# Kernel optimization log

Measured on AMD Instinct MI355X. Metric: run time of the kernel, lower is better.

## Reference

```python
import jax, jax.numpy as jnp
import numpy as np

N, P, E, HID = 20000, 12, 640000, 100

def setup_inputs() -> dict:
    key = jax.random.key(0)
    ks = jax.random.split(key, 20)
    inp = {}
    inp['x'] = jax.random.normal(ks[0], (N, P), dtype=jnp.float32)
    inp['edge_index'] = jax.random.randint(ks[1], (2, E), 0, N, dtype=jnp.int64)
    inp['edge_weight'] = jax.random.uniform(ks[2], (E,), dtype=jnp.float32)
    s = 0.1
    # GCNConv weights (in=1, out=HID) and biases for z, r, h gates
    inp['W_z'] = jax.random.normal(ks[3], (1, HID)) * s
    inp['b_z'] = jnp.zeros((HID,))
    inp['W_r'] = jax.random.normal(ks[4], (1, HID)) * s
    inp['b_r'] = jnp.zeros((HID,))
    inp['W_h'] = jax.random.normal(ks[5], (1, HID)) * s
    inp['b_h'] = jnp.zeros((HID,))
    # TGCN linear layers: Linear(2*HID, HID), stored as (in, out)
    inp['Wl_z'] = jax.random.normal(ks[6], (2 * HID, HID)) * s
    inp['bl_z'] = jnp.zeros((HID,))
    inp['Wl_r'] = jax.random.normal(ks[7], (2 * HID, HID)) * s
    inp['bl_r'] = jnp.zeros((HID,))
    inp['Wl_h'] = jax.random.normal(ks[8], (2 * HID, HID)) * s
    inp['bl_h'] = jnp.zeros((HID,))
    # A3TGCN temporal attention logits over periods
    inp['att'] = jax.random.uniform(ks[9], (P,))
    # final Linear(100, 1)
    inp['W_out'] = jax.random.normal(ks[10], (HID, 1)) * s
    inp['b_out'] = jnp.zeros((1,))
    return inp

def _gcn_aggregate(x_np, edge_index, edge_weight):
    # symmetric GCN normalization with self-loops (PyG gcn_norm), then
    # aggregate neighbor features: out[i] = sum_j norm_ij * x[j]
    n = x_np.shape[0]
    src, dst = edge_index[0], edge_index[1]
    loop = jnp.arange(n)
    s = jnp.concatenate([src, loop])
    d = jnp.concatenate([dst, loop])
    w = jnp.concatenate([edge_weight, jnp.ones((n,), dtype=x_np.dtype)])
    deg = jax.ops.segment_sum(w, d, num_segments=n)
    dinv = jnp.where(deg > 0, deg ** -0.5, 0.0)
    norm = dinv[s] * w * dinv[d]                      # (E+N,)
    msgs = norm[:, None] * x_np[s]                    # (E+N, P)
    return jax.ops.segment_sum(msgs, d, num_segments=n)  # (N, P)

def reference(x, edge_index, edge_weight, W_z, b_z, W_r, b_r, W_h, b_h,
              Wl_z, bl_z, Wl_r, bl_r, Wl_h, bl_h, att, W_out, b_out):
    # x: (N, P) -> viewed as (N, in_channels=1, P) in the torch module.
    # GCNConv is linear in x, so aggregate once and apply each gate's weight.
    agg = _gcn_aggregate(x, edge_index, edge_weight)       # (N, P)
    C_z = agg[:, :, None] * W_z[0] + b_z                   # (N, P, HID)
    C_r = agg[:, :, None] * W_r[0] + b_r
    C_h = agg[:, :, None] * W_h[0] + b_h
    # A3TGCN calls TGCN with H=None (zeros) for every period independently.
    H0 = jnp.zeros_like(C_z)
    Z = jax.nn.sigmoid(jnp.concatenate([C_z, H0], -1) @ Wl_z + bl_z)
    R = jax.nn.sigmoid(jnp.concatenate([C_r, H0], -1) @ Wl_r + bl_r)
    Ht = jnp.tanh(jnp.concatenate([C_h, H0 * R], -1) @ Wl_h + bl_h)
    Hp = Z * H0 + (1.0 - Z) * Ht                           # (N, P, HID)
    probs = jax.nn.softmax(att)                            # (P,)
    H_acc = jnp.einsum('npo,p->no', Hp, probs)             # (N, HID)
    h = jax.nn.relu(H_acc)
    return h @ W_out + b_out                               # (N, 1)
```

## Files before the change

kernel.cpp:

```cpp
#include <hip/hip_runtime.h>
#include <hip/hip_bf16.h>

constexpr int N_NODES = 20000;
constexpr int P_PER   = 12;
constexpr int N_EDGES = 640000;
constexpr int HID     = 100;
constexpr int CAP     = 80;

constexpr size_t OFF_DINV   = 0;
constexpr size_t OFF_UZ     = OFF_DINV + N_NODES;
constexpr size_t OFF_CZ     = OFF_UZ + HID;
constexpr size_t OFF_UH     = OFF_CZ + HID;
constexpr size_t OFF_CH     = OFF_UH + HID;
constexpr size_t OFF_PROBS  = OFF_CH + HID;
constexpr size_t OFF_CNT    = OFF_PROBS + P_PER;
constexpr size_t OFF_BUCKET = OFF_CNT + N_NODES;

__global__ void precompute_kernel(const float* __restrict__ Wz, const float* __restrict__ bz,
                                  const float* __restrict__ Wh, const float* __restrict__ bh,
                                  const float* __restrict__ Wlz, const float* __restrict__ blz,
                                  const float* __restrict__ Wlh, const float* __restrict__ blh,
                                  const float* __restrict__ att,
                                  float* __restrict__ uz, float* __restrict__ cz,
                                  float* __restrict__ uh, float* __restrict__ ch,
                                  float* __restrict__ probs) {
    int t = threadIdx.x;
    if (t < HID) {
        float suz = 0.f, scz = 0.f, suh = 0.f, sch = 0.f;
        for (int j = 0; j < HID; ++j) {
            float wlz = Wlz[j * HID + t];
            float wlh = Wlh[j * HID + t];
            suz += Wz[j] * wlz;
            scz += bz[j] * wlz;
            suh += Wh[j] * wlh;
            sch += bh[j] * wlh;
        }
        uz[t] = suz;
        cz[t] = scz + blz[t];
        uh[t] = suh;
        ch[t] = sch + blh[t];
    }
    if (t == 0) {
        float m = att[0];
        for (int p = 1; p < P_PER; ++p) m = fmaxf(m, att[p]);
        float e[P_PER];
        float s = 0.f;
        for (int p = 0; p < P_PER; ++p) { e[p] = __expf(att[p] - m); s += e[p]; }
        float inv = 1.0f / s;
        for (int p = 0; p < P_PER; ++p) probs[p] = e[p] * inv;
    }
}

__global__ void fill_bucket_kernel(const int* __restrict__ ei, const float* __restrict__ w,
                                   int* __restrict__ cnt, int2* __restrict__ bucket) {
    int e = blockIdx.x * blockDim.x + threadIdx.x;
    if (e >= N_EDGES) return;
    int s = ei[e];
    int d = ei[N_EDGES + e];
    float wt = w[e];
    int pos = atomicAdd(cnt + d, 1);
    if (pos < CAP) bucket[(size_t)d * CAP + pos] = make_int2(s, __float_as_int(wt));
}

__global__ void degdinv_kernel(const int2* __restrict__ bucket, const int* __restrict__ cnt,
                               float* __restrict__ dinv) {
    int tid = blockIdx.x * blockDim.x + threadIdx.x;
    int n = tid >> 4;
    int l = tid & 15;
    if (n >= N_NODES) return;
    int c = min(cnt[n], CAP);
    const int2* row = bucket + (size_t)n * CAP;
    float s = 0.f;
    for (int j = l; j < c; j += 16) s += __int_as_float(row[j].y);
#pragma unroll
    for (int off = 8; off >= 1; off >>= 1) s += __shfl_xor(s, off, 64);
    if (l == 0) dinv[n] = rsqrtf(1.0f + s);
}

__global__ void gather_finalize_kernel(const int2* __restrict__ bucket, const int* __restrict__ cnt,
                                       const float* __restrict__ x, const float* __restrict__ dinv,
                                       const float* __restrict__ uz, const float* __restrict__ cz,
                                       const float* __restrict__ uh, const float* __restrict__ ch,
                                       const float* __restrict__ probs,
                                       const float* __restrict__ Wout, const float* __restrict__ bout,
                                       float* __restrict__ out) {
    __shared__ float s_uz[HID], s_cz[HID], s_uh[HID], s_ch[HID], s_wo[HID];
    __shared__ float s_pr[P_PER];
    int t = threadIdx.x;
    if (t < HID) {
        s_uz[t] = uz[t]; s_cz[t] = cz[t];
        s_uh[t] = uh[t]; s_ch[t] = ch[t];
        s_wo[t] = Wout[t];
    }
    if (t < P_PER) s_pr[t] = probs[t];
    __syncthreads();

    int tid = blockIdx.x * blockDim.x + t;
    int n = tid >> 4;
    int l = tid & 15;
    if (n >= N_NODES) return;

    int c = min(cnt[n], CAP);
    float dn = dinv[n];
    const int2* row = bucket + (size_t)n * CAP;

    float acc[P_PER];
#pragma unroll
    for (int p = 0; p < P_PER; ++p) acc[p] = 0.f;
    for (int j = l; j < c; j += 16) {
        int2 ent = row[j];
        int s = ent.x;
        float norm = dinv[s] * __int_as_float(ent.y) * dn;
        const float4* xr = (const float4*)(x + (size_t)s * P_PER);
        float4 x0 = xr[0], x1 = xr[1], x2 = xr[2];
        acc[0]  += norm * x0.x;  acc[1]  += norm * x0.y;
        acc[2]  += norm * x0.z;  acc[3]  += norm * x0.w;
        acc[4]  += norm * x1.x;  acc[5]  += norm * x1.y;
        acc[6]  += norm * x1.z;  acc[7]  += norm * x1.w;
        acc[8]  += norm * x2.x;  acc[9]  += norm * x2.y;
        acc[10] += norm * x2.z;  acc[11] += norm * x2.w;
    }
#pragma unroll
    for (int off = 8; off >= 1; off >>= 1) {
#pragma unroll
        for (int p = 0; p < P_PER; ++p) acc[p] += __shfl_xor(acc[p], off, 64);
    }
    {
        const float4* xr = (const float4*)(x + (size_t)n * P_PER);
        float4 x0 = xr[0], x1 = xr[1], x2 = xr[2];
        float self = dn * dn;
        acc[0]  += self * x0.x;  acc[1]  += self * x0.y;
        acc[2]  += self * x0.z;  acc[3]  += self * x0.w;
        acc[4]  += self * x1.x;  acc[5]  += self * x1.y;
        acc[6]  += self * x1.z;  acc[7]  += self * x1.w;
        acc[8]  += self * x2.x;  acc[9]  += self * x2.y;
        acc[10] += self * x2.z;  acc[11] += self * x2.w;
    }
    float rk = 0.f;
    for (int k = l; k < HID; k += 16) {
        float uzk = s_uz[k], czk = s_cz[k], uhk = s_uh[k], chk = s_ch[k];
        float a2 = 0.f;
#pragma unroll
        for (int p = 0; p < P_PER; ++p) {
            float a  = acc[p];
            float vz = fminf(fmaxf(a * uzk + czk, -30.f), 30.f);
            float vh = fminf(fmaxf(a * uhk + chk, -15.f), 15.f);
            float ez  = __expf(vz);
            float e2h = __expf(2.0f * vh);
            float term = (e2h - 1.0f) / ((1.0f + ez) * (e2h + 1.0f));
            a2 += s_pr[p] * term;
        }
        rk += fmaxf(a2, 0.0f) * s_wo[k];
    }
#pragma unroll
    for (int off = 8; off >= 1; off >>= 1) rk += __shfl_xor(rk, off, 64);
    if (l == 0) out[n] = rk + bout[0];
}

extern "C" void kernel_launch(void* const* d_in, const int* in_sizes, int n_in,
                              void* d_out, int out_size, void* d_ws, size_t ws_size,
                              hipStream_t stream) {
    const float* x   = (const float*)d_in[0];
    const int*   ei  = (const int*)d_in[1];
    const float* ew  = (const float*)d_in[2];
    const float* Wz  = (const float*)d_in[3];
    const float* bz  = (const float*)d_in[4];
    const float* Wh  = (const float*)d_in[7];
    const float* bh  = (const float*)d_in[8];
    const float* Wlz = (const float*)d_in[9];
    const float* blz = (const float*)d_in[10];
    const float* Wlh = (const float*)d_in[13];
    const float* blh = (const float*)d_in[14];
    const float* att = (const float*)d_in[15];
    const float* Wout = (const float*)d_in[16];
    const float* bout = (const float*)d_in[17];
    float* out = (float*)d_out;

    float* ws    = (float*)d_ws;
    float* dinv  = ws + OFF_DINV;
    float* uz    = ws + OFF_UZ;
    float* cz    = ws + OFF_CZ;
    float* uh    = ws + OFF_UH;
    float* ch    = ws + OFF_CH;
    float* probs = ws + OFF_PROBS;
    int*   cnt   = (int*)(ws + OFF_CNT);
    int2*  bucket = (int2*)(ws + OFF_BUCKET);

    hipMemsetAsync(cnt, 0, N_NODES * sizeof(int), stream);
    hipLaunchKernelGGL(precompute_kernel, dim3(1), dim3(128), 0, stream,
                       Wz, bz, Wh, bh, Wlz, blz, Wlh, blh, att, uz, cz, uh, ch, probs);
    hipLaunchKernelGGL(fill_bucket_kernel, dim3((N_EDGES + 255) / 256), dim3(256), 0, stream,
                       ei, ew, cnt, bucket);
    hipLaunchKernelGGL(degdinv_kernel, dim3((N_NODES * 16 + 255) / 256), dim3(256), 0, stream,
                       bucket, cnt, dinv);
    hipLaunchKernelGGL(gather_finalize_kernel, dim3((N_NODES * 16 + 255) / 256), dim3(256), 0, stream,
                       bucket, cnt, x, dinv, uz, cz, uh, ch, probs, Wout, bout, out);
}
```

Before: 168.3 us.

## Prescale node features by dinv and pad atomic counters to reduce contention

```diff
diff --git a/kernel.cpp b/kernel.cpp
--- a/kernel.cpp
+++ b/kernel.cpp
@@ -6,6 +6,8 @@
 constexpr int N_EDGES = 640000;
 constexpr int HID     = 100;
 constexpr int CAP     = 80;
+constexpr int CNT_STR = 16;
+constexpr int Y_STR   = 16;
 
 constexpr size_t OFF_DINV   = 0;
 constexpr size_t OFF_UZ     = OFF_DINV + N_NODES;
@@ -13,8 +15,9 @@
 constexpr size_t OFF_UH     = OFF_CZ + HID;
 constexpr size_t OFF_CH     = OFF_UH + HID;
 constexpr size_t OFF_PROBS  = OFF_CH + HID;
-constexpr size_t OFF_CNT    = OFF_PROBS + P_PER;
-constexpr size_t OFF_BUCKET = OFF_CNT + N_NODES;
+constexpr size_t OFF_CNT    = 20416;
+constexpr size_t OFF_Y      = OFF_CNT + (size_t)N_NODES * CNT_STR;
+constexpr size_t OFF_BUCKET = OFF_Y + (size_t)N_NODES * Y_STR;
 
 __global__ void precompute_kernel(const float* __restrict__ Wz, const float* __restrict__ bz,
                                   const float* __restrict__ Wh, const float* __restrict__ bh,
@@ -58,27 +61,30 @@
     int s = ei[e];
     int d = ei[N_EDGES + e];
     float wt = w[e];
-    int pos = atomicAdd(cnt + d, 1);
+    int pos = atomicAdd(cnt + (size_t)d * CNT_STR, 1);
     if (pos < CAP) bucket[(size_t)d * CAP + pos] = make_int2(s, __float_as_int(wt));
 }
 
-__global__ void degdinv_kernel(const int2* __restrict__ bucket, const int* __restrict__ cnt,
-                               float* __restrict__ dinv) {
+__global__ void degdinv_y_kernel(const int2* __restrict__ bucket, const int* __restrict__ cnt,
+                                 const float* __restrict__ x,
+                                 float* __restrict__ dinv, float* __restrict__ y) {
     int tid = blockIdx.x * blockDim.x + threadIdx.x;
     int n = tid >> 4;
     int l = tid & 15;
     if (n >= N_NODES) return;
-    int c = min(cnt[n], CAP);
+    int c = min(cnt[(size_t)n * CNT_STR], CAP);
     const int2* row = bucket + (size_t)n * CAP;
     float s = 0.f;
     for (int j = l; j < c; j += 16) s += __int_as_float(row[j].y);
 #pragma unroll
     for (int off = 8; off >= 1; off >>= 1) s += __shfl_xor(s, off, 64);
-    if (l == 0) dinv[n] = rsqrtf(1.0f + s);
+    float dv = rsqrtf(1.0f + s);
+    if (l == 0) dinv[n] = dv;
+    if (l < P_PER) y[(size_t)n * Y_STR + l] = dv * x[(size_t)n * P_PER + l];
 }
 
 __global__ void gather_finalize_kernel(const int2* __restrict__ bucket, const int* __restrict__ cnt,
-                                       const float* __restrict__ x, const float* __restrict__ dinv,
+                                       const float* __restrict__ y, const float* __restrict__ dinv,
                                        const float* __restrict__ uz, const float* __restrict__ cz,
                                        const float* __restrict__ uh, const float* __restrict__ ch,
                                        const float* __restrict__ probs,
@@ -100,8 +106,7 @@
     int l = tid & 15;
     if (n >= N_NODES) return;
 
-    int c = min(cnt[n], CAP);
-    float dn = dinv[n];
+    int c = min(cnt[(size_t)n * CNT_STR], CAP);
     const int2* row = bucket + (size_t)n * CAP;
 
     float acc[P_PER];
@@ -109,16 +114,15 @@
     for (int p = 0; p < P_PER; ++p) acc[p] = 0.f;
     for (int j = l; j < c; j += 16) {
         int2 ent = row[j];
-        int s = ent.x;
-        float norm = dinv[s] * __int_as_float(ent.y) * dn;
-        const float4* xr = (const float4*)(x + (size_t)s * P_PER);
-        float4 x0 = xr[0], x1 = xr[1], x2 = xr[2];
-        acc[0]  += norm * x0.x;  acc[1]  += norm * x0.y;
-        acc[2]  += norm * x0.z;  acc[3]  += norm * x0.w;
-        acc[4]  += norm * x1.x;  acc[5]  += norm * x1.y;
-        acc[6]  += norm * x1.z;  acc[7]  += norm * x1.w;
-        acc[8]  += norm * x2.x;  acc[9]  += norm * x2.y;
-        acc[10] += norm * x2.z;  acc[11] += norm * x2.w;
+        float wt = __int_as_float(ent.y);
+        const float4* yr = (const float4*)(y + (size_t)ent.x * Y_STR);
+        float4 y0 = yr[0], y1 = yr[1], y2 = yr[2];
+        acc[0]  += wt * y0.x;  acc[1]  += wt * y0.y;
+        acc[2]  += wt * y0.z;  acc[3]  += wt * y0.w;
+        acc[4]  += wt * y1.x;  acc[5]  += wt * y1.y;
+        acc[6]  += wt * y1.z;  acc[7]  += wt * y1.w;
+        acc[8]  += wt * y2.x;  acc[9]  += wt * y2.y;
+        acc[10] += wt * y2.z;  acc[11] += wt * y2.w;
     }
 #pragma unroll
     for (int off = 8; off >= 1; off >>= 1) {
@@ -126,15 +130,15 @@
         for (int p = 0; p < P_PER; ++p) acc[p] += __shfl_xor(acc[p], off, 64);
     }
     {
-        const float4* xr = (const float4*)(x + (size_t)n * P_PER);
-        float4 x0 = xr[0], x1 = xr[1], x2 = xr[2];
-        float self = dn * dn;
-        acc[0]  += self * x0.x;  acc[1]  += self * x0.y;
-        acc[2]  += self * x0.z;  acc[3]  += self * x0.w;
-        acc[4]  += self * x1.x;  acc[5]  += self * x1.y;
-        acc[6]  += self * x1.z;  acc[7]  += self * x1.w;
-        acc[8]  += self * x2.x;  acc[9]  += self * x2.y;
-        acc[10] += self * x2.z;  acc[11] += self * x2.w;
+        float dn = dinv[n];
+        const float4* yr = (const float4*)(y + (size_t)n * Y_STR);
+        float4 y0 = yr[0], y1 = yr[1], y2 = yr[2];
+        acc[0]  = dn * (acc[0]  + y0.x);  acc[1]  = dn * (acc[1]  + y0.y);
+        acc[2]  = dn * (acc[2]  + y0.z);  acc[3]  = dn * (acc[3]  + y0.w);
+        acc[4]  = dn * (acc[4]  + y1.x);  acc[5]  = dn * (acc[5]  + y1.y);
+        acc[6]  = dn * (acc[6]  + y1.z);  acc[7]  = dn * (acc[7]  + y1.w);
+        acc[8]  = dn * (acc[8]  + y2.x);  acc[9]  = dn * (acc[9]  + y2.y);
+        acc[10] = dn * (acc[10] + y2.z);  acc[11] = dn * (acc[11] + y2.w);
     }
     float rk = 0.f;
     for (int k = l; k < HID; k += 16) {
@@ -176,23 +180,24 @@
     const float* bout = (const float*)d_in[17];
     float* out = (float*)d_out;
 
-    float* ws    = (float*)d_ws;
-    float* dinv  = ws + OFF_DINV;
-    float* uz    = ws + OFF_UZ;
-    float* cz    = ws + OFF_CZ;
-    float* uh    = ws + OFF_UH;
-    float* ch    = ws + OFF_CH;
-    float* probs = ws + OFF_PROBS;
-    int*   cnt   = (int*)(ws + OFF_CNT);
+    float* ws     = (float*)d_ws;
+    float* dinv   = ws + OFF_DINV;
+    float* uz     = ws + OFF_UZ;
+    float* cz     = ws + OFF_CZ;
+    float* uh     = ws + OFF_UH;
+    float* ch     = ws + OFF_CH;
+    float* probs  = ws + OFF_PROBS;
+    int*   cnt    = (int*)(ws + OFF_CNT);
+    float* y      = ws + OFF_Y;
     int2*  bucket = (int2*)(ws + OFF_BUCKET);
 
-    hipMemsetAsync(cnt, 0, N_NODES * sizeof(int), stream);
+    hipMemsetAsync(cnt, 0, (size_t)N_NODES * CNT_STR * sizeof(int), stream);
     hipLaunchKernelGGL(precompute_kernel, dim3(1), dim3(128), 0, stream,
                        Wz, bz, Wh, bh, Wlz, blz, Wlh, blh, att, uz, cz, uh, ch, probs);
     hipLaunchKernelGGL(fill_bucket_kernel, dim3((N_EDGES + 255) / 256), dim3(256), 0, stream,
                        ei, ew, cnt, bucket);
-    hipLaunchKernelGGL(degdinv_kernel, dim3((N_NODES * 16 + 255) / 256), dim3(256), 0, stream,
-                       bucket, cnt, dinv);
+    hipLaunchKernelGGL(degdinv_y_kernel, dim3((N_NODES * 16 + 255) / 256), dim3(256), 0, stream,
+                       bucket, cnt, x, dinv, y);
     hipLaunchKernelGGL(gather_finalize_kernel, dim3((N_NODES * 16 + 255) / 256), dim3(256), 0, stream,
-                       bucket, cnt, x, dinv, uz, cz, uh, ch, probs, Wout, bout, out);
-}
+                       bucket, cnt, y, dinv, uz, cz, uh, ch, probs, Wout, bout, out);
+}
```

Result: faster. 161.2 us (-4.2%).

## Partition edges into 64-node destination bins with block-local LDS aggregation

Applied to the files above, without the earlier changes.

```diff
diff --git a/kernel.cpp b/kernel.cpp
--- a/kernel.cpp
+++ b/kernel.cpp
@@ -5,16 +5,24 @@
 constexpr int P_PER   = 12;
 constexpr int N_EDGES = 640000;
 constexpr int HID     = 100;
-constexpr int CAP     = 80;
-
-constexpr size_t OFF_DINV   = 0;
-constexpr size_t OFF_UZ     = OFF_DINV + N_NODES;
-constexpr size_t OFF_CZ     = OFF_UZ + HID;
-constexpr size_t OFF_UH     = OFF_CZ + HID;
-constexpr size_t OFF_CH     = OFF_UH + HID;
-constexpr size_t OFF_PROBS  = OFF_CH + HID;
-constexpr size_t OFF_CNT    = OFF_PROBS + P_PER;
-constexpr size_t OFF_BUCKET = OFF_CNT + N_NODES;
+
+constexpr int BIN_W   = 64;
+constexpr int NB      = (N_NODES + BIN_W - 1) / BIN_W;
+constexpr int BCAP    = 2560;
+constexpr int NBLK2   = 160;
+constexpr int CHUNK   = N_EDGES / NBLK2;
+constexpr int CUR_STR = 16;
+constexpr int Y_STR   = 16;
+
+constexpr size_t OFF_DINV  = 0;
+constexpr size_t OFF_UZ    = OFF_DINV + N_NODES;
+constexpr size_t OFF_CZ    = OFF_UZ + HID;
+constexpr size_t OFF_UH    = OFF_CZ + HID;
+constexpr size_t OFF_CH    = OFF_UH + HID;
+constexpr size_t OFF_PROBS = OFF_CH + HID;
+constexpr size_t OFF_CUR   = 20416;
+constexpr size_t OFF_Y     = OFF_CUR + (size_t)NB * CUR_STR;
+constexpr size_t OFF_SEG   = OFF_Y + (size_t)N_NODES * Y_STR;
 
 __global__ void precompute_kernel(const float* __restrict__ Wz, const float* __restrict__ bz,
                                   const float* __restrict__ Wh, const float* __restrict__ bh,
@@ -51,41 +59,82 @@
     }
 }
 
-__global__ void fill_bucket_kernel(const int* __restrict__ ei, const float* __restrict__ w,
-                                   int* __restrict__ cnt, int2* __restrict__ bucket) {
-    int e = blockIdx.x * blockDim.x + threadIdx.x;
-    if (e >= N_EDGES) return;
-    int s = ei[e];
-    int d = ei[N_EDGES + e];
-    float wt = w[e];
-    int pos = atomicAdd(cnt + d, 1);
-    if (pos < CAP) bucket[(size_t)d * CAP + pos] = make_int2(s, __float_as_int(wt));
-}
-
-__global__ void degdinv_kernel(const int2* __restrict__ bucket, const int* __restrict__ cnt,
-                               float* __restrict__ dinv) {
-    int tid = blockIdx.x * blockDim.x + threadIdx.x;
-    int n = tid >> 4;
-    int l = tid & 15;
-    if (n >= N_NODES) return;
-    int c = min(cnt[n], CAP);
-    const int2* row = bucket + (size_t)n * CAP;
-    float s = 0.f;
-    for (int j = l; j < c; j += 16) s += __int_as_float(row[j].y);
-#pragma unroll
-    for (int off = 8; off >= 1; off >>= 1) s += __shfl_xor(s, off, 64);
-    if (l == 0) dinv[n] = rsqrtf(1.0f + s);
-}
-
-__global__ void gather_finalize_kernel(const int2* __restrict__ bucket, const int* __restrict__ cnt,
-                                       const float* __restrict__ x, const float* __restrict__ dinv,
-                                       const float* __restrict__ uz, const float* __restrict__ cz,
-                                       const float* __restrict__ uh, const float* __restrict__ ch,
-                                       const float* __restrict__ probs,
-                                       const float* __restrict__ Wout, const float* __restrict__ bout,
-                                       float* __restrict__ out) {
+__global__ __launch_bounds__(256) void partition_kernel(const int* __restrict__ ei,
+                                                        const float* __restrict__ w,
+                                                        int* __restrict__ cur,
+                                                        int2* __restrict__ seg) {
+    __shared__ int hist[NB];
+    __shared__ int base[NB];
+    __shared__ int run[NB];
+    int t = threadIdx.x;
+    for (int b = t; b < NB; b += 256) { hist[b] = 0; run[b] = 0; }
+    __syncthreads();
+    int e0 = blockIdx.x * CHUNK;
+    const int* __restrict__ dsts = ei + N_EDGES;
+    for (int i = t; i < CHUNK; i += 256) {
+        int d = dsts[e0 + i];
+        atomicAdd(&hist[d >> 6], 1);
+    }
+    __syncthreads();
+    for (int b = t; b < NB; b += 256) {
+        int h = hist[b];
+        base[b] = (h > 0) ? atomicAdd(cur + (size_t)b * CUR_STR, h) : 0;
+    }
+    __syncthreads();
+    for (int i = t; i < CHUNK; i += 256) {
+        int s = ei[e0 + i];
+        int d = dsts[e0 + i];
+        float wt = w[e0 + i];
+        int b = d >> 6;
+        int pos = base[b] + atomicAdd(&run[b], 1);
+        if (pos < BCAP)
+            seg[(size_t)b * BCAP + pos] = make_int2(s | ((d & 63) << 16), __float_as_int(wt));
+    }
+}
+
+__global__ __launch_bounds__(256) void degdinv_y_kernel(const int2* __restrict__ seg,
+                                                        const int* __restrict__ cur,
+                                                        const float* __restrict__ x,
+                                                        float* __restrict__ dinv,
+                                                        float* __restrict__ y) {
+    __shared__ float wsum[BIN_W];
+    int t = threadIdx.x;
+    int b = blockIdx.x;
+    if (t < BIN_W) wsum[t] = 0.f;
+    __syncthreads();
+    int c = min(cur[(size_t)b * CUR_STR], BCAP);
+    const int2* sg = seg + (size_t)b * BCAP;
+    for (int i = t; i < c; i += 256) {
+        int2 e = sg[i];
+        atomicAdd(&wsum[e.x >> 16], __int_as_float(e.y));
+    }
+    __syncthreads();
+    if (t < BIN_W) wsum[t] = rsqrtf(1.0f + wsum[t]);
+    __syncthreads();
+    int n0 = b * BIN_W;
+    if (t < BIN_W && n0 + t < N_NODES) dinv[n0 + t] = wsum[t];
+    for (int i = t; i < BIN_W * P_PER; i += 256) {
+        int nl = i / P_PER, p = i - nl * P_PER;
+        int n = n0 + nl;
+        if (n < N_NODES) y[(size_t)n * Y_STR + p] = wsum[nl] * x[(size_t)n * P_PER + p];
+    }
+}
+
+__global__ __launch_bounds__(256) void gather_finalize_kernel(const int2* __restrict__ seg,
+                                                              const int* __restrict__ cur,
+                                                              const float* __restrict__ y,
+                                                              const float* __restrict__ dinv,
+                                                              const float* __restrict__ uz,
+                                                              const float* __restrict__ cz,
+                                                              const float* __restrict__ uh,
+                                                              const float* __restrict__ ch,
+                                                              const float* __restrict__ probs,
+                                                              const float* __restrict__ Wout,
+                                                              const float* __restrict__ bout,
+                                                              float* __restrict__ out) {
     __shared__ float s_uz[HID], s_cz[HID], s_uh[HID], s_ch[HID], s_wo[HID];
     __shared__ float s_pr[P_PER];
+    __shared__ float agg[BIN_W][P_PER + 1];
     int t = threadIdx.x;
     if (t < HID) {
         s_uz[t] = uz[t]; s_cz[t] = cz[t];
@@ -93,58 +142,53 @@
         s_wo[t] = Wout[t];
     }
     if (t < P_PER) s_pr[t] = probs[t];
-    __syncthreads();
-
-    int tid = blockIdx.x * blockDim.x + t;
-    int n = tid >> 4;
-    int l = tid & 15;
+    for (int i = t; i < BIN_W * (P_PER + 1); i += 256) ((float*)agg)[i] = 0.f;
+    __syncthreads();
+
+    int b = blockIdx.x;
+    int c = min(cur[(size_t)b * CUR_STR], BCAP);
+    const int2* sg = seg + (size_t)b * BCAP;
+    for (int i = t; i < c; i += 256) {
+        int2 e = sg[i];
+        int s  = e.x & 0xFFFF;
+        int dl = e.x >> 16;
+        float wt = __int_as_float(e.y);
+        const float4* yr = (const float4*)(y + (size_t)s * Y_STR);
+        float4 y0 = yr[0], y1 = yr[1], y2 = yr[2];
+        atomicAdd(&agg[dl][0],  wt * y0.x);  atomicAdd(&agg[dl][1],  wt * y0.y);
+        atomicAdd(&agg[dl][2],  wt * y0.z);  atomicAdd(&agg[dl][3],  wt * y0.w);
+        atomicAdd(&agg[dl][4],  wt * y1.x);  atomicAdd(&agg[dl][5],  wt * y1.y);
+        atomicAdd(&agg[dl][6],  wt * y1.z);  atomicAdd(&agg[dl][7],  wt * y1.w);
+        atomicAdd(&agg[dl][8],  wt * y2.x);  atomicAdd(&agg[dl][9],  wt * y2.y);
+        atomicAdd(&agg[dl][10], wt * y2.z);  atomicAdd(&agg[dl][11], wt * y2.w);
+    }
+    __syncthreads();
+
+    int nl = t >> 2;
+    int l  = t & 3;
+    int n  = b * BIN_W + nl;
     if (n >= N_NODES) return;
-
-    int c = min(cnt[n], CAP);
     float dn = dinv[n];
-    const int2* row = bucket + (size_t)n * CAP;
-
-    float acc[P_PER];
-#pragma unroll
-    for (int p = 0; p < P_PER; ++p) acc[p] = 0.f;
-    for (int j = l; j < c; j += 16) {
-        int2 ent = row[j];
-        int s = ent.x;
-        float norm = dinv[s] * __int_as_float(ent.y) * dn;
-        const float4* xr = (const float4*)(x + (size_t)s * P_PER);
-        float4 x0 = xr[0], x1 = xr[1], x2 = xr[2];
-        acc[0]  += norm * x0.x;  acc[1]  += norm * x0.y;
-        acc[2]  += norm * x0.z;  acc[3]  += norm * x0.w;
-        acc[4]  += norm * x1.x;  acc[5]  += norm * x1.y;
-        acc[6]  += norm * x1.z;  acc[7]  += norm * x1.w;
-        acc[8]  += norm * x2.x;  acc[9]  += norm * x2.y;
-        acc[10] += norm * x2.z;  acc[11] += norm * x2.w;
-    }
-#pragma unroll
-    for (int off = 8; off >= 1; off >>= 1) {
-#pragma unroll
-        for (int p = 0; p < P_PER; ++p) acc[p] += __shfl_xor(acc[p], off, 64);
-    }
+    float a[P_PER];
     {
-        const float4* xr = (const float4*)(x + (size_t)n * P_PER);
-        float4 x0 = xr[0], x1 = xr[1], x2 = xr[2];
-        float self = dn * dn;
-        acc[0]  += self * x0.x;  acc[1]  += self * x0.y;
-        acc[2]  += self * x0.z;  acc[3]  += self * x0.w;
-        acc[4]  += self * x1.x;  acc[5]  += self * x1.y;
-        acc[6]  += self * x1.z;  acc[7]  += self * x1.w;
-        acc[8]  += self * x2.x;  acc[9]  += self * x2.y;
-        acc[10] += self * x2.z;  acc[11] += self * x2.w;
+        const float4* yr = (const float4*)(y + (size_t)n * Y_STR);
+        float4 y0 = yr[0], y1 = yr[1], y2 = yr[2];
+        a[0]  = dn * (agg[nl][0]  + y0.x);  a[1]  = dn * (agg[nl][1]  + y0.y);
+        a[2]  = dn * (agg[nl][2]  + y0.z);  a[3]  = dn * (agg[nl][3]  + y0.w);
+        a[4]  = dn * (agg[nl][4]  + y1.x);  a[5]  = dn * (agg[nl][5]  + y1.y);
+        a[6]  = dn * (agg[nl][6]  + y1.z);  a[7]  = dn * (agg[nl][7]  + y1.w);
+        a[8]  = dn * (agg[nl][8]  + y2.x);  a[9]  = dn * (agg[nl][9]  + y2.y);
+        a[10] = dn * (agg[nl][10] + y2.z);  a[11] = dn * (agg[nl][11] + y2.w);
     }
     float rk = 0.f;
-    for (int k = l; k < HID; k += 16) {
+    for (int k = l; k < HID; k += 4) {
         float uzk = s_uz[k], czk = s_cz[k], uhk = s_uh[k], chk = s_ch[k];
         float a2 = 0.f;
 #pragma unroll
         for (int p = 0; p < P_PER; ++p) {
-            float a  = acc[p];
-            float vz = fminf(fmaxf(a * uzk + czk, -30.f), 30.f);
-            float vh = fminf(fmaxf(a * uhk + chk, -15.f), 15.f);
+            float av = a[p];
+            float vz = fminf(fmaxf(av * uzk + czk, -30.f), 30.f);
+            float vh = fminf(fmaxf(av * uhk + chk, -15.f), 15.f);
             float ez  = __expf(vz);
             float e2h = __expf(2.0f * vh);
             float term = (e2h - 1.0f) / ((1.0f + ez) * (e2h + 1.0f));
@@ -152,8 +196,8 @@
         }
         rk += fmaxf(a2, 0.0f) * s_wo[k];
     }
-#pragma unroll
-    for (int off = 8; off >= 1; off >>= 1) rk += __shfl_xor(rk, off, 64);
+    rk += __shfl_xor(rk, 1, 64);
+    rk += __shfl_xor(rk, 2, 64);
     if (l == 0) out[n] = rk + bout[0];
 }
 
@@ -183,16 +227,17 @@
     float* uh    = ws + OFF_UH;
     float* ch    = ws + OFF_CH;
     float* probs = ws + OFF_PROBS;
-    int*   cnt   = (int*)(ws + OFF_CNT);
-    int2*  bucket = (int2*)(ws + OFF_BUCKET);
-
-    hipMemsetAsync(cnt, 0, N_NODES * sizeof(int), stream);
+    int*   cur   = (int*)(ws + OFF_CUR);
+    float* y     = ws + OFF_Y;
+    int2*  seg   = (int2*)(ws + OFF_SEG);
+
+    hipMemsetAsync(cur, 0, (size_t)NB * CUR_STR * sizeof(int), stream);
     hipLaunchKernelGGL(precompute_kernel, dim3(1), dim3(128), 0, stream,
                        Wz, bz, Wh, bh, Wlz, blz, Wlh, blh, att, uz, cz, uh, ch, probs);
-    hipLaunchKernelGGL(fill_bucket_kernel, dim3((N_EDGES + 255) / 256), dim3(256), 0, stream,
-                       ei, ew, cnt, bucket);
-    hipLaunchKernelGGL(degdinv_kernel, dim3((N_NODES * 16 + 255) / 256), dim3(256), 0, stream,
-                       bucket, cnt, dinv);
-    hipLaunchKernelGGL(gather_finalize_kernel, dim3((N_NODES * 16 + 255) / 256), dim3(256), 0, stream,
-                       bucket, cnt, x, dinv, uz, cz, uh, ch, probs, Wout, bout, out);
-}
+    hipLaunchKernelGGL(partition_kernel, dim3(NBLK2), dim3(256), 0, stream,
+                       ei, ew, cur, seg);
+    hipLaunchKernelGGL(degdinv_y_kernel, dim3(NB), dim3(256), 0, stream,
+                       seg, cur, x, dinv, y);
+    hipLaunchKernelGGL(gather_finalize_kernel, dim3(NB), dim3(256), 0, stream,
+                       seg, cur, y, dinv, uz, cz, uh, ch, probs, Wout, bout, out);
+}
```

New measurement: 221.1 us. 1.31x slower.
